# Performance work log

Hardware: AMD Instinct MI355X
Metric: run time of the kernel (lower is better)

Reference implementation:

```python
import jax, jax.numpy as jnp
import numpy as np

# layer config (init kwargs)
ZERO_SCALE = 0.25
MAX_WIDTH = 5
BASE = 2
START_AT_ONE = False
N_SCALES = 4  # = input_shape[-2]


def _scale_params():
    # scales = (base**i - 1) * zero_scale, i = 1..n_scales (start_at_one=False)
    scales = [float(BASE ** i - 1) * ZERO_SCALE for i in range(1, N_SCALES + 1)]
    widths = [int(MAX_WIDTH * s) for s in scales]  # tf.cast -> truncation
    # base 1D filter: -(linspace(-w,w,2w+1)**2) / scale**2, shape (2w+1,)
    fbases = [
        (-(np.linspace(-w, w, 2 * w + 1).astype(np.float32) ** 2) / np.float32(s * s))
        for w, s in zip(widths, scales)
    ]
    return scales, widths, fbases


def _morph1d(x, taps, axis, dilate):
    """Separable 1D max-plus (dilation) / min-minus (erosion) along `axis`.

    x: (B, H, W, C); taps: (L, C); VALID: output dim = in - L + 1.
    TF dilation2d: max_j x[p+j] + f[j]; TF erosion2d: min_j x[p+j] - f[j]
    (filter is symmetric so the TF filter reversal is a no-op).
    """
    L = taps.shape[0]
    n = x.shape[axis] - L + 1
    sl = lambda j: jax.lax.slice_in_dim(x, j, j + n, axis=axis)
    if dilate:
        out = sl(0) + taps[0]
        for j in range(1, L):
            out = jnp.maximum(out, sl(j) + taps[j])
    else:
        out = sl(0) - taps[0]
        for j in range(1, L):
            out = jnp.minimum(out, sl(j) - taps[j])
    return out


def setup_inputs() -> dict:
    key = jax.random.key(0)
    k1, k2, k3, k4 = jax.random.split(key, 4)
    B, H, W, S, C = 8, 192, 192, N_SCALES, 32
    x = jax.random.normal(k1, (B, H, W, S, C), dtype=jnp.float32)
    # constraints: coef >= 1/max_width**2, c >= 1, alpha in [0,1]
    coef = 0.5 + jax.random.uniform(k2, (1, C), dtype=jnp.float32)
    c = 1.0 + jax.random.uniform(k3, (1, 1, C), dtype=jnp.float32)
    alpha = jax.random.uniform(k4, (1, 1, 1, C), dtype=jnp.float32)
    return {"x": x, "coef": coef, "c": c, "alpha": alpha}


def reference(x, coef, c, alpha):
    _, widths, fbases = _scale_params()
    c_lc = c[0]  # (1, C), broadcasts against (L, C) taps
    outs = []
    for i in range(N_SCALES):
        k = jnp.asarray(fbases[i])[:, None] * coef  # (L,1)*(1,C) -> (L,C)
        kc = k * c_lc                                # (L,C)
        s = widths[i]
        x0 = x[..., i, :]                            # (B,H,W,C)
        # edge padding by 2s on both spatial dims
        x0 = jnp.pad(x0, ((0, 0), (2 * s, 2 * s), (2 * s, 2 * s), (0, 0)), mode="edge")
        # closing: dilate(kx), dilate(ky), erode(kx*c), erode(ky*c)
        xc = _morph1d(x0, k, 1, True)
        xc = _morph1d(xc, k, 2, True)
        xc = _morph1d(xc, kc, 1, False)
        xc = _morph1d(xc, kc, 2, False)
        # opening: erode(kx), erode(ky), dilate(kx*c), dilate(ky*c)
        xo = _morph1d(x0, k, 1, False)
        xo = _morph1d(xo, k, 2, False)
        xo = _morph1d(xo, kc, 1, True)
        xo = _morph1d(xo, kc, 2, True)
        outs.append(alpha * xc + (1.0 - alpha) * xo)  # (B,H,W,C)
    return jnp.stack(outs, -2)  # (B,H,W,n_scales,C)
```

## Files before the change

### kernel.cpp

```cpp
#include <hip/hip_runtime.h>


constexpr int BB = 8, HH = 192, WW = 192, CHN = 32, SCST = 128;

constexpr float s2_of(int si) {
    return si == 0 ? 0.0625f : si == 1 ? 0.5625f : si == 2 ? 3.0625f : 14.0625f;
}
constexpr int cdiv_(int a, int b) { return (a + b - 1) / b; }

template <int SI, int SW, int NH, int MW>
__launch_bounds__(512, MW) __global__
void k_hpass1(const float* __restrict__ x, const float* __restrict__ coef,
              float* __restrict__ A, float* __restrict__ Bb) {
    constexpr int L = 2 * SW + 1, HA = HH + 2 * SW, WN = NH + 2 * SW;
    constexpr float S2 = s2_of(SI);
    const int tid = threadIdx.x;
    const int c = tid & 31, wl = tid >> 5;
    const int w0 = blockIdx.x * 16;
    const int r0 = blockIdx.y * NH;
    const int b  = blockIdx.z;
    const float kmul = coef[c];

    float wb[WN];
    const float* xb = x + ((size_t)(b * HH) * WW + (w0 + wl)) * SCST + SI * CHN + c;
#pragma unroll
    for (int t = 0; t < WN; ++t) {
        int gh = r0 + t - 2 * SW;
        gh = gh < 0 ? 0 : (gh > HH - 1 ? HH - 1 : gh);
        wb[t] = xb[(size_t)gh * (WW * SCST)];
    }

    __shared__ float stg[NH][CHN][17];
    const int c2 = tid >> 4, w2 = tid & 15;

    {
        float acc[NH];
#pragma unroll
        for (int j = 0; j < L; ++j) {
            float v = (float)(j - SW);
            float tp = (-(v * v) / S2) * kmul;
#pragma unroll
            for (int o = 0; o < NH; ++o) {
                float t = wb[o + j] + tp;
                acc[o] = (j == 0) ? t : fmaxf(acc[o], t);
            }
        }
#pragma unroll
        for (int o = 0; o < NH; ++o) stg[o][c][wl] = acc[o];
    }
    __syncthreads();
#pragma unroll
    for (int o = 0; o < NH; ++o) {
        int r = r0 + o;
        if (r < HA) A[((size_t)(c2 * BB + b) * HA + r) * WW + w0 + w2] = stg[o][c2][w2];
    }
    __syncthreads();
    {
        float acc[NH];
#pragma unroll
        for (int j = 0; j < L; ++j) {
            float v = (float)(j - SW);
            float tp = (-(v * v) / S2) * kmul;
#pragma unroll
            for (int o = 0; o < NH; ++o) {
                float t = wb[o + j] - tp;
                acc[o] = (j == 0) ? t : fminf(acc[o], t);
            }
        }
#pragma unroll
        for (int o = 0; o < NH; ++o) stg[o][c][wl] = acc[o];
    }
    __syncthreads();
#pragma unroll
    for (int o = 0; o < NH; ++o) {
        int r = r0 + o;
        if (r < HA) Bb[((size_t)(c2 * BB + b) * HA + r) * WW + w0 + w2] = stg[o][c2][w2];
    }
}

template <int SI, int SW, int BR>
__launch_bounds__(256, 4) __global__
void k_wpass2(float* __restrict__ P, const float* __restrict__ coef,
              const float* __restrict__ cin) {
    constexpr int L = 2 * SW + 1, HA = HH + 2 * SW, WE = WW + 2 * SW;
    constexpr int NQ1 = cdiv_(WE, 32), NQ2 = WW / 32;
    constexpr float S2 = s2_of(SI);
    __shared__ float inb[8][WW + 1];
    __shared__ float tmp[8][WE + 1];
    const int tid = threadIdx.x;
    const int rl = tid >> 5, l = tid & 31;
    const size_t row = (size_t)blockIdx.x * 8 + rl;
    float* Prow = P + row * WW;
    const int c = (int)(row / (size_t)(BB * HA));
    const float k1 = coef[c], k2 = coef[c] * cin[c];

    for (int i = l; i < WW; i += 32) inb[rl][i] = Prow[i];
    __syncthreads();
    {
        const int q0 = l * NQ1;
        float wbuf[NQ1 + 2 * SW];
#pragma unroll
        for (int t = 0; t < NQ1 + 2 * SW; ++t) {
            int idx = q0 + t - 2 * SW;
            idx = idx < 0 ? 0 : (idx > WW - 1 ? WW - 1 : idx);
            wbuf[t] = inb[rl][idx];
        }
        float acc[NQ1];
#pragma unroll
        for (int j = 0; j < L; ++j) {
            float v = (float)(j - SW);
            float tp = (-(v * v) / S2) * k1;
#pragma unroll
            for (int o = 0; o < NQ1; ++o) {
                float t = (BR == 0) ? wbuf[o + j] + tp : wbuf[o + j] - tp;
                acc[o] = (j == 0) ? t : ((BR == 0) ? fmaxf(acc[o], t) : fminf(acc[o], t));
            }
        }
#pragma unroll
        for (int o = 0; o < NQ1; ++o) {
            int q = q0 + o;
            if (q < WE) tmp[rl][q] = acc[o];
        }
    }
    __syncthreads();
    {
        const int q0 = l * NQ2;
        float wbuf[NQ2 + 2 * SW];
#pragma unroll
        for (int t = 0; t < NQ2 + 2 * SW; ++t) wbuf[t] = tmp[rl][q0 + t];
        float acc[NQ2];
#pragma unroll
        for (int j = 0; j < L; ++j) {
            float v = (float)(j - SW);
            float tp = (-(v * v) / S2) * k2;
#pragma unroll
            for (int o = 0; o < NQ2; ++o) {
                float t = (BR == 0) ? wbuf[o + j] - tp : wbuf[o + j] + tp;
                acc[o] = (j == 0) ? t : ((BR == 0) ? fminf(acc[o], t) : fmaxf(acc[o], t));
            }
        }
#pragma unroll
        for (int o = 0; o < NQ2; ++o) Prow[q0 + o] = acc[o];
    }
}

template <int SI, int SW, int MW>
__launch_bounds__(256, MW) __global__
void k_hpass3(const float* __restrict__ A, const float* __restrict__ Bb,
              const float* __restrict__ coef, const float* __restrict__ cin,
              const float* __restrict__ ain, float* __restrict__ res) {
    constexpr int L = 2 * SW + 1, HA = HH + 2 * SW, RS = 64, RT = RS + 2 * SW;
    constexpr float S2 = s2_of(SI);
    __shared__ float tile[RT][64 + 1];
    const int tid = threadIdx.x;
    const int p = blockIdx.z;
    const int c = p >> 3;
    const int w0 = blockIdx.x * 64, r0 = blockIdx.y * RS;
    const float kc = coef[c] * cin[c], av = ain[c];
    const int wl = tid & 63, rq = tid >> 6;

    const float* Ab = A + ((size_t)p * HA + r0) * WW + w0;
    for (int i = tid; i < RT * 64; i += 256) {
        int r = i >> 6, w = i & 63;
        tile[r][w] = Ab[(size_t)r * WW + w];
    }
    __syncthreads();
    float xc[16];
    {
        float wbuf[16 + 2 * SW];
#pragma unroll
        for (int t = 0; t < 16 + 2 * SW; ++t) wbuf[t] = tile[rq * 16 + t][wl];
#pragma unroll
        for (int j = 0; j < L; ++j) {
            float v = (float)(j - SW);
            float tp = (-(v * v) / S2) * kc;
#pragma unroll
            for (int o = 0; o < 16; ++o) {
                float t = wbuf[o + j] - tp;
                xc[o] = (j == 0) ? t : fminf(xc[o], t);
            }
        }
    }
    __syncthreads();
    const float* Bp = Bb + ((size_t)p * HA + r0) * WW + w0;
    for (int i = tid; i < RT * 64; i += 256) {
        int r = i >> 6, w = i & 63;
        tile[r][w] = Bp[(size_t)r * WW + w];
    }
    __syncthreads();
    float outv[16];
    {
        float wbuf[16 + 2 * SW];
#pragma unroll
        for (int t = 0; t < 16 + 2 * SW; ++t) wbuf[t] = tile[rq * 16 + t][wl];
        float xo[16];
#pragma unroll
        for (int j = 0; j < L; ++j) {
            float v = (float)(j - SW);
            float tp = (-(v * v) / S2) * kc;
#pragma unroll
            for (int o = 0; o < 16; ++o) {
                float t = wbuf[o + j] + tp;
                xo[o] = (j == 0) ? t : fmaxf(xo[o], t);
            }
        }
#pragma unroll
        for (int o = 0; o < 16; ++o) outv[o] = av * xc[o] + (1.0f - av) * xo[o];
    }
    float* rp = res + ((size_t)p * HH + r0) * WW + w0;
#pragma unroll
    for (int o = 0; o < 16; ++o) rp[(size_t)(rq * 16 + o) * WW + wl] = outv[o];
}

template <int SI>
__launch_bounds__(256, 8) __global__
void k_scatter(const float* __restrict__ res, float* __restrict__ out) {
    __shared__ float stg[CHN][33];
    const int tid = threadIdx.x;
    const int w0 = blockIdx.x * 32, h = blockIdx.y, b = blockIdx.z;
#pragma unroll
    for (int it = 0; it < 4; ++it) {
        int cc = (tid >> 5) + it * 8, w = tid & 31;
        stg[cc][w] = res[((size_t)(cc * BB + b) * HH + h) * WW + w0 + w];
    }
    __syncthreads();
#pragma unroll
    for (int it = 0; it < 4; ++it) {
        int w = (tid >> 5) + it * 8, cc = tid & 31;
        out[((size_t)(b * HH + h) * WW + w0 + w) * SCST + SI * CHN + cc] = stg[cc][w];
    }
}

constexpr int r4_(int a) { return (a + 3) & ~3; }
constexpr int pickNH(int R, int C, int NT) {
    for (int nh = 1; nh <= R; ++nh)
        if (cdiv_(R, nh) * C <= NT) return nh;
    return R;
}
template <int L, int SW, int SI, bool DIL, int NH, int R, int PIT>
__device__ __forceinline__ void pass_compute_si(const float* __restrict__ in, int r0, int c,
                                                float kmul, float (&acc)[NH]) {
    constexpr float S2 = s2_of(SI);
    float wb[NH + L - 1];
#pragma unroll
    for (int t = 0; t < NH + L - 1; ++t) {
        int rr = r0 + t;
        if (rr > R + L - 2) rr = R + L - 2;
        wb[t] = in[rr * PIT + c];
    }
#pragma unroll
    for (int j = 0; j < L; ++j) {
        float v = (float)(j - SW);
        float tp = (-(v * v) / S2) * kmul;
#pragma unroll
        for (int o = 0; o < NH; ++o) {
            float t = DIL ? wb[o + j] + tp : wb[o + j] - tp;
            if (j == 0) acc[o] = t;
            else acc[o] = DIL ? fmaxf(acc[o], t) : fminf(acc[o], t);
        }
    }
}
template <int L, int SW, int SI, bool DIL, int NH, int R, int C, int PIT, int POUT, int NT>
__device__ __forceinline__ void pass_lds(const float* __restrict__ in, float* __restrict__ outT,
                                         float kmul, int tid) {
    constexpr int nseg = cdiv_(R, NH);
    for (int item = tid; item < nseg * C; item += NT) {
        int c = item % C, r0 = (item / C) * NH;
        float acc[NH];
        pass_compute_si<L, SW, SI, DIL, NH, R, PIT>(in, r0, c, kmul, acc);
#pragma unroll
        for (int o = 0; o < NH; ++o)
            if (r0 + o < R) outT[c * POUT + (r0 + o)] = acc[o];
    }
}
template <int SI, int SW, int TH, int TW, int NT, int MW>
__launch_bounds__(NT, MW) __global__
void lasry_kernel(const float* __restrict__ x, const float* __restrict__ coef,
                  const float* __restrict__ cin, const float* __restrict__ ain,
                  float* __restrict__ out) {
    constexpr int L = 2 * SW + 1;
    constexpr int IH = TH + 4 * SW, IW = TW + 4 * SW;
    constexpr int R1 = TH + 2 * SW, C1 = IW;
    constexpr int R2 = TW + 2 * SW, C2 = R1;
    constexpr int R3 = TH,          C3 = R2;
    constexpr int R4 = TW,          C4 = R3;
    constexpr int PIN = IW, PA = r4_(R1), PB = r4_(R2), PA2 = r4_(R3);
    constexpr int NH1 = pickNH(R1, C1, NT), NH2 = pickNH(R2, C2, NT);
    constexpr int NH3 = pickNH(R3, C3, NT), NH4 = pickNH(R4, C4, NT);
    __shared__ float smem[IH * PIN + C1 * PA + C2 * PB];
    float* bufIn = smem;
    float* A = smem + IH * PIN;
    float* B = A + C1 * PA;
    float* A2 = A;
    const int tid = threadIdx.x;
    const int b = blockIdx.z >> 5, ch = blockIdx.z & 31;
    const int h0 = blockIdx.y * TH, w0 = blockIdx.x * TW;
    const float kmul = coef[ch];
    const float kcmul = kmul * cin[ch];
    const float av = ain[ch];
    const float* xb = x + (size_t)(b * HH * WW) * SCST + SI * CHN + ch;
    constexpr int NLOAD = cdiv_(IH * IW, NT);
#pragma unroll
    for (int t = 0; t < NLOAD; ++t) {
        int idx = tid + t * NT;
        if (idx < IH * IW) {
            int r = idx / IW, c = idx - r * IW;
            int gh = min(max(h0 + r - 2 * SW, 0), HH - 1);
            int gw = min(max(w0 + c - 2 * SW, 0), WW - 1);
            bufIn[r * PIN + c] = xb[(size_t)(gh * WW + gw) * SCST];
        }
    }
    __syncthreads();
    const int c4 = tid % C4;
    const int r04 = (tid / C4) * NH4;
    const bool act4 = tid < cdiv_(R4, NH4) * C4;
    float xcv[NH4];
    pass_lds<L, SW, SI, true,  NH1, R1, C1, PIN, PA,  NT>(bufIn, A, kmul, tid);  __syncthreads();
    pass_lds<L, SW, SI, true,  NH2, R2, C2, PA,  PB,  NT>(A,     B, kmul, tid);  __syncthreads();
    pass_lds<L, SW, SI, false, NH3, R3, C3, PB,  PA2, NT>(B,    A2, kcmul, tid); __syncthreads();
    if (act4) pass_compute_si<L, SW, SI, false, NH4, R4, PA2>(A2, r04, c4, kcmul, xcv);
    __syncthreads();
    pass_lds<L, SW, SI, false, NH1, R1, C1, PIN, PA,  NT>(bufIn, A, kmul, tid);  __syncthreads();
    pass_lds<L, SW, SI, false, NH2, R2, C2, PA,  PB,  NT>(A,     B, kmul, tid);  __syncthreads();
    pass_lds<L, SW, SI, true,  NH3, R3, C3, PB,  PA2, NT>(B,    A2, kcmul, tid); __syncthreads();
    if (act4) {
        float xov[NH4];
        pass_compute_si<L, SW, SI, true, NH4, R4, PA2>(A2, r04, c4, kcmul, xov);
        const int h = h0 + c4;
        float* ob = out + ((size_t)(b * HH + h) * WW) * SCST + SI * CHN + ch;
#pragma unroll
        for (int o = 0; o < NH4; ++o) {
            int w = w0 + r04 + o;
            if (r04 + o < R4 && w < WW) ob[(size_t)w * SCST] = av * xcv[o] + (1.0f - av) * xov[o];
        }
    }
}

template <int SI, int SW, int NH, int MW1>
static void launch_scale(const float* x, const float* coef, const float* cv, const float* av,
                         float* out, float* A, float* Bb, float* res, hipStream_t stream) {
    constexpr int HA = HH + 2 * SW;
    k_hpass1<SI, SW, NH, MW1><<<dim3(WW / 16, cdiv_(HA, NH), BB), 512, 0, stream>>>(x, coef, A, Bb);
    k_wpass2<SI, SW, 0><<<dim3(CHN * BB * HA / 8), 256, 0, stream>>>(A, coef, cv);
    k_wpass2<SI, SW, 1><<<dim3(CHN * BB * HA / 8), 256, 0, stream>>>(Bb, coef, cv);
    k_hpass3<SI, SW, 4><<<dim3(WW / 64, HH / 64, CHN * BB), 256, 0, stream>>>(A, Bb, coef, cv, av, res);
    k_scatter<SI><<<dim3(WW / 32, HH, BB), 256, 0, stream>>>(res, out);
}

extern "C" void kernel_launch(void* const* d_in, const int* in_sizes, int n_in,
                              void* d_out, int out_size, void* d_ws, size_t ws_size,
                              hipStream_t stream) {
    const float* x    = (const float*)d_in[0];
    const float* coef = (const float*)d_in[1];
    const float* cv   = (const float*)d_in[2];
    const float* av   = (const float*)d_in[3];
    float* out = (float*)d_out;
    (void)in_sizes; (void)n_in; (void)out_size;

    constexpr size_t BUFSZ = (size_t)CHN * BB * 228 * WW;
    constexpr size_t RESSZ = (size_t)CHN * BB * HH * WW;
    constexpr size_t WS_NEED = (2 * BUFSZ + RESSZ) * sizeof(float);

    if (ws_size >= WS_NEED) {
        float* A   = (float*)d_ws;
        float* Bb  = A + BUFSZ;
        float* res = A + 2 * BUFSZ;
        launch_scale<0, 1, 14, 4>(x, coef, cv, av, out, A, Bb, res, stream);
        launch_scale<1, 3, 18, 4>(x, coef, cv, av, out, A, Bb, res, stream);
        launch_scale<2, 8, 24, 4>(x, coef, cv, av, out, A, Bb, res, stream);
        launch_scale<3, 18, 24, 3>(x, coef, cv, av, out, A, Bb, res, stream);
    } else {
        lasry_kernel<0, 1, 64, 64, 1024, 8><<<dim3(3, 3, 256), 1024, 0, stream>>>(x, coef, cv, av, out);
        lasry_kernel<1, 3, 64, 64, 1024, 8><<<dim3(3, 3, 256), 1024, 0, stream>>>(x, coef, cv, av, out);
        lasry_kernel<2, 8, 64, 64, 1024, 4><<<dim3(3, 3, 256), 1024, 0, stream>>>(x, coef, cv, av, out);
        lasry_kernel<3, 18, 64, 48, 1024, 4><<<dim3(4, 3, 256), 1024, 0, stream>>>(x, coef, cv, av, out);
    }
}
```

Measured before the change: 759.0 us.

## Interleave channels in intermediates, merge wpass launches, fuse hpass3 with output scatter

Changes the intermediate buffer layout from channel-major to (b, row, channel, w) so the final vertical pass can read all 32 channels of a strip and write the interleaved output directly. This removes the separate res buffer and the scatter kernel. The two width-pass launches are merged into one grid with a y-dimension branch, and that pass now uses float4 loads and stores with an LDS staging writeback. Strip heights and occupancy hints are retuned per scale, at the cost of more register pressure in the new fused kernel.

```diff
diff --git a/kernel.cpp b/kernel.cpp
--- a/kernel.cpp
+++ b/kernel.cpp
@@ -52,7 +52,7 @@
 #pragma unroll
     for (int o = 0; o < NH; ++o) {
         int r = r0 + o;
-        if (r < HA) A[((size_t)(c2 * BB + b) * HA + r) * WW + w0 + w2] = stg[o][c2][w2];
+        if (r < HA) A[((size_t)(b * HA + r) * CHN + c2) * WW + w0 + w2] = stg[o][c2][w2];
     }
     __syncthreads();
     {
@@ -74,27 +74,30 @@
 #pragma unroll
     for (int o = 0; o < NH; ++o) {
         int r = r0 + o;
-        if (r < HA) Bb[((size_t)(c2 * BB + b) * HA + r) * WW + w0 + w2] = stg[o][c2][w2];
+        if (r < HA) Bb[((size_t)(b * HA + r) * CHN + c2) * WW + w0 + w2] = stg[o][c2][w2];
     }
 }
 
 template <int SI, int SW, int BR>
-__launch_bounds__(256, 4) __global__
-void k_wpass2(float* __restrict__ P, const float* __restrict__ coef,
-              const float* __restrict__ cin) {
-    constexpr int L = 2 * SW + 1, HA = HH + 2 * SW, WE = WW + 2 * SW;
+__device__ __forceinline__ void wpass_body(float* __restrict__ P, const float* __restrict__ coef,
+                                           const float* __restrict__ cin) {
+    constexpr int L = 2 * SW + 1, WE = WW + 2 * SW;
     constexpr int NQ1 = cdiv_(WE, 32), NQ2 = WW / 32;
     constexpr float S2 = s2_of(SI);
-    __shared__ float inb[8][WW + 1];
-    __shared__ float tmp[8][WE + 1];
+    __shared__ float inb[8][200];
+    __shared__ float tmp[8][((WE + 3) & ~3) + 4];
     const int tid = threadIdx.x;
     const int rl = tid >> 5, l = tid & 31;
     const size_t row = (size_t)blockIdx.x * 8 + rl;
     float* Prow = P + row * WW;
-    const int c = (int)(row / (size_t)(BB * HA));
+    const int c = (int)(row & 31);
     const float k1 = coef[c], k2 = coef[c] * cin[c];
 
-    for (int i = l; i < WW; i += 32) inb[rl][i] = Prow[i];
+#pragma unroll
+    for (int i = 0; i < 2; ++i) {
+        int q = l + i * 32;
+        if (q < 48) ((float4*)&inb[rl][0])[q] = ((const float4*)Prow)[q];
+    }
     __syncthreads();
     {
         const int q0 = l * NQ1;
@@ -140,95 +143,86 @@
             }
         }
 #pragma unroll
-        for (int o = 0; o < NQ2; ++o) Prow[q0 + o] = acc[o];
-    }
-}
-
-template <int SI, int SW, int MW>
-__launch_bounds__(256, MW) __global__
-void k_hpass3(const float* __restrict__ A, const float* __restrict__ Bb,
-              const float* __restrict__ coef, const float* __restrict__ cin,
-              const float* __restrict__ ain, float* __restrict__ res) {
-    constexpr int L = 2 * SW + 1, HA = HH + 2 * SW, RS = 64, RT = RS + 2 * SW;
+        for (int o = 0; o < NQ2; ++o) inb[rl][q0 + o] = acc[o];
+    }
+    __syncthreads();
+#pragma unroll
+    for (int i = 0; i < 2; ++i) {
+        int q = l + i * 32;
+        if (q < 48) ((float4*)Prow)[q] = ((float4*)&inb[rl][0])[q];
+    }
+}
+
+template <int SI, int SW>
+__launch_bounds__(256, 8) __global__
+void k_wpass2(float* __restrict__ A, float* __restrict__ Bb,
+              const float* __restrict__ coef, const float* __restrict__ cin) {
+    if (blockIdx.y == 0) wpass_body<SI, SW, 0>(A, coef, cin);
+    else                 wpass_body<SI, SW, 1>(Bb, coef, cin);
+}
+
+template <int SI, int SW, int NH, int MW>
+__launch_bounds__(512, MW) __global__
+void k_fin3(const float* __restrict__ A, const float* __restrict__ Bb,
+            const float* __restrict__ coef, const float* __restrict__ cin,
+            const float* __restrict__ ain, float* __restrict__ out) {
+    constexpr int L = 2 * SW + 1, HA = HH + 2 * SW, WN = NH + 2 * SW;
     constexpr float S2 = s2_of(SI);
-    __shared__ float tile[RT][64 + 1];
+    static_assert(HH % NH == 0, "no partial strips");
     const int tid = threadIdx.x;
-    const int p = blockIdx.z;
-    const int c = p >> 3;
-    const int w0 = blockIdx.x * 64, r0 = blockIdx.y * RS;
+    const int c = tid >> 4, w = tid & 15;
+    const int w0 = blockIdx.x * 16;
+    const int h0 = blockIdx.y * NH;
+    const int b  = blockIdx.z;
     const float kc = coef[c] * cin[c], av = ain[c];
-    const int wl = tid & 63, rq = tid >> 6;
-
-    const float* Ab = A + ((size_t)p * HA + r0) * WW + w0;
-    for (int i = tid; i < RT * 64; i += 256) {
-        int r = i >> 6, w = i & 63;
-        tile[r][w] = Ab[(size_t)r * WW + w];
-    }
-    __syncthreads();
-    float xc[16];
-    {
-        float wbuf[16 + 2 * SW];
-#pragma unroll
-        for (int t = 0; t < 16 + 2 * SW; ++t) wbuf[t] = tile[rq * 16 + t][wl];
+
+    __shared__ float stg[NH][CHN][17];
+
+    {
+        float wb[WN];
+#pragma unroll
+        for (int t = 0; t < WN; ++t)
+            wb[t] = A[((size_t)(b * HA + h0 + t) * CHN + c) * WW + w0 + w];
+        float acc[NH];
 #pragma unroll
         for (int j = 0; j < L; ++j) {
             float v = (float)(j - SW);
             float tp = (-(v * v) / S2) * kc;
 #pragma unroll
-            for (int o = 0; o < 16; ++o) {
-                float t = wbuf[o + j] - tp;
-                xc[o] = (j == 0) ? t : fminf(xc[o], t);
-            }
-        }
-    }
-    __syncthreads();
-    const float* Bp = Bb + ((size_t)p * HA + r0) * WW + w0;
-    for (int i = tid; i < RT * 64; i += 256) {
-        int r = i >> 6, w = i & 63;
-        tile[r][w] = Bp[(size_t)r * WW + w];
-    }
-    __syncthreads();
-    float outv[16];
-    {
-        float wbuf[16 + 2 * SW];
-#pragma unroll
-        for (int t = 0; t < 16 + 2 * SW; ++t) wbuf[t] = tile[rq * 16 + t][wl];
-        float xo[16];
+            for (int o = 0; o < NH; ++o) {
+                float t = wb[o + j] - tp;
+                acc[o] = (j == 0) ? t : fminf(acc[o], t);
+            }
+        }
+#pragma unroll
+        for (int o = 0; o < NH; ++o) stg[o][c][w] = acc[o];
+    }
+    {
+        float wb[WN];
+#pragma unroll
+        for (int t = 0; t < WN; ++t)
+            wb[t] = Bb[((size_t)(b * HA + h0 + t) * CHN + c) * WW + w0 + w];
+        float acc[NH];
 #pragma unroll
         for (int j = 0; j < L; ++j) {
             float v = (float)(j - SW);
             float tp = (-(v * v) / S2) * kc;
 #pragma unroll
-            for (int o = 0; o < 16; ++o) {
-                float t = wbuf[o + j] + tp;
-                xo[o] = (j == 0) ? t : fmaxf(xo[o], t);
-            }
-        }
-#pragma unroll
-        for (int o = 0; o < 16; ++o) outv[o] = av * xc[o] + (1.0f - av) * xo[o];
-    }
-    float* rp = res + ((size_t)p * HH + r0) * WW + w0;
-#pragma unroll
-    for (int o = 0; o < 16; ++o) rp[(size_t)(rq * 16 + o) * WW + wl] = outv[o];
-}
-
-template <int SI>
-__launch_bounds__(256, 8) __global__
-void k_scatter(const float* __restrict__ res, float* __restrict__ out) {
-    __shared__ float stg[CHN][33];
-    const int tid = threadIdx.x;
-    const int w0 = blockIdx.x * 32, h = blockIdx.y, b = blockIdx.z;
-#pragma unroll
-    for (int it = 0; it < 4; ++it) {
-        int cc = (tid >> 5) + it * 8, w = tid & 31;
-        stg[cc][w] = res[((size_t)(cc * BB + b) * HH + h) * WW + w0 + w];
-    }
-    __syncthreads();
-#pragma unroll
-    for (int it = 0; it < 4; ++it) {
-        int w = (tid >> 5) + it * 8, cc = tid & 31;
-        out[((size_t)(b * HH + h) * WW + w0 + w) * SCST + SI * CHN + cc] = stg[cc][w];
-    }
+            for (int o = 0; o < NH; ++o) {
+                float t = wb[o + j] + tp;
+                acc[o] = (j == 0) ? t : fmaxf(acc[o], t);
+            }
+        }
+#pragma unroll
+        for (int o = 0; o < NH; ++o)
+            stg[o][c][w] = av * stg[o][c][w] + (1.0f - av) * acc[o];
+    }
+    __syncthreads();
+    const int c2 = tid & 31, w2 = tid >> 5;
+    float* ob = out + SI * CHN + c2;
+#pragma unroll
+    for (int o = 0; o < NH; ++o)
+        ob[((size_t)(b * HH + h0 + o) * WW + w0 + w2) * SCST] = stg[o][c2][w2];
 }
 
 constexpr int r4_(int a) { return (a + 3) & ~3; }
@@ -336,15 +330,13 @@
     }
 }
 
-template <int SI, int SW, int NH, int MW1>
+template <int SI, int SW, int NH1, int MW1, int NH3, int MW3>
 static void launch_scale(const float* x, const float* coef, const float* cv, const float* av,
-                         float* out, float* A, float* Bb, float* res, hipStream_t stream) {
+                         float* out, float* A, float* Bb, hipStream_t stream) {
     constexpr int HA = HH + 2 * SW;
-    k_hpass1<SI, SW, NH, MW1><<<dim3(WW / 16, cdiv_(HA, NH), BB), 512, 0, stream>>>(x, coef, A, Bb);
-    k_wpass2<SI, SW, 0><<<dim3(CHN * BB * HA / 8), 256, 0, stream>>>(A, coef, cv);
-    k_wpass2<SI, SW, 1><<<dim3(CHN * BB * HA / 8), 256, 0, stream>>>(Bb, coef, cv);
-    k_hpass3<SI, SW, 4><<<dim3(WW / 64, HH / 64, CHN * BB), 256, 0, stream>>>(A, Bb, coef, cv, av, res);
-    k_scatter<SI><<<dim3(WW / 32, HH, BB), 256, 0, stream>>>(res, out);
+    k_hpass1<SI, SW, NH1, MW1><<<dim3(WW / 16, cdiv_(HA, NH1), BB), 512, 0, stream>>>(x, coef, A, Bb);
+    k_wpass2<SI, SW><<<dim3(BB * HA * CHN / 8, 2), 256, 0, stream>>>(A, Bb, coef, cv);
+    k_fin3<SI, SW, NH3, MW3><<<dim3(WW / 16, HH / NH3, BB), 512, 0, stream>>>(A, Bb, coef, cv, av, out);
 }
 
 extern "C" void kernel_launch(void* const* d_in, const int* in_sizes, int n_in,
@@ -357,18 +349,16 @@
     float* out = (float*)d_out;
     (void)in_sizes; (void)n_in; (void)out_size;
 
-    constexpr size_t BUFSZ = (size_t)CHN * BB * 228 * WW;
-    constexpr size_t RESSZ = (size_t)CHN * BB * HH * WW;
-    constexpr size_t WS_NEED = (2 * BUFSZ + RESSZ) * sizeof(float);
+    constexpr size_t BUFSZ = (size_t)BB * 228 * CHN * WW;
+    constexpr size_t WS_NEED = 2 * BUFSZ * sizeof(float);
 
     if (ws_size >= WS_NEED) {
-        float* A   = (float*)d_ws;
-        float* Bb  = A + BUFSZ;
-        float* res = A + 2 * BUFSZ;
-        launch_scale<0, 1, 14, 4>(x, coef, cv, av, out, A, Bb, res, stream);
-        launch_scale<1, 3, 18, 4>(x, coef, cv, av, out, A, Bb, res, stream);
-        launch_scale<2, 8, 24, 4>(x, coef, cv, av, out, A, Bb, res, stream);
-        launch_scale<3, 18, 24, 3>(x, coef, cv, av, out, A, Bb, res, stream);
+        float* A  = (float*)d_ws;
+        float* Bb = A + BUFSZ;
+        launch_scale<0, 1,  24, 4, 24, 4>(x, coef, cv, av, out, A, Bb, stream);
+        launch_scale<1, 3,  24, 4, 24, 4>(x, coef, cv, av, out, A, Bb, stream);
+        launch_scale<2, 8,  24, 3, 32, 3>(x, coef, cv, av, out, A, Bb, stream);
+        launch_scale<3, 18, 24, 3, 32, 3>(x, coef, cv, av, out, A, Bb, stream);
     } else {
         lasry_kernel<0, 1, 64, 64, 1024, 8><<<dim3(3, 3, 256), 1024, 0, stream>>>(x, coef, cv, av, out);
         lasry_kernel<1, 3, 64, 64, 1024, 8><<<dim3(3, 3, 256), 1024, 0, stream>>>(x, coef, cv, av, out);
```

New measurement: 865.7 us. 14.1% more time.
